# Optimization experiments

Hardware: AMD Instinct MI355X
Metric: run time of the kernel (lower is better)

Reference implementation:

```python
import jax, jax.numpy as jnp
import numpy as np

B, S, H, NH = 8, 512, 768, 12
HD = H // NH  # 64


def setup_inputs() -> dict:
    key = jax.random.key(0)
    ks = jax.random.split(key, 8)
    scale = 0.02
    return {
        "hidden_states": jax.random.normal(ks[0], (B, S, H), dtype=jnp.float32),
        "attention_mask": jnp.zeros((B, 1, 1, S), dtype=jnp.float32),
        "Wq": jax.random.normal(ks[1], (H, H), dtype=jnp.float32) * scale,
        "bq": jnp.zeros((H,), dtype=jnp.float32),
        "Wk": jax.random.normal(ks[2], (H, H), dtype=jnp.float32) * scale,
        "bk": jnp.zeros((H,), dtype=jnp.float32),
        "Wv": jax.random.normal(ks[3], (H, H), dtype=jnp.float32) * scale,
        "bv": jnp.zeros((H,), dtype=jnp.float32),
    }


def reference(hidden_states, attention_mask, Wq, bq, Wk, bk, Wv, bv):
    # BERT-style self-attention (dropout disabled / eval mode).
    def heads(x):  # [B,S,H] -> [B,NH,S,HD]
        return x.reshape(B, S, NH, HD).transpose(0, 2, 1, 3)

    q = heads(hidden_states @ Wq.T + bq)
    k = heads(hidden_states @ Wk.T + bk)
    v = heads(hidden_states @ Wv.T + bv)

    scores = jnp.einsum("bnqd,bnkd->bnqk", q, k) / jnp.sqrt(jnp.float32(HD))
    scores = scores + attention_mask  # additive mask broadcast over heads/queries
    probs = jax.nn.softmax(scores, axis=-1)
    ctx = jnp.einsum("bnqk,bnkd->bnqd", probs, v)
    return ctx.transpose(0, 2, 1, 3).reshape(B, S, H)
```

## Files before the change

kernel.cpp:

```cpp
#include <hip/hip_runtime.h>
#include <hip/hip_bf16.h>

typedef __bf16 bf16x8 __attribute__((ext_vector_type(8)));
typedef float f32x4 __attribute__((ext_vector_type(4)));
typedef float f32x16 __attribute__((ext_vector_type(16)));
typedef unsigned int u32x2 __attribute__((ext_vector_type(2)));
typedef unsigned int u32x4 __attribute__((ext_vector_type(4)));
typedef unsigned short us8 __attribute__((ext_vector_type(8)));

#define MFMA32(a, b, c) __builtin_amdgcn_mfma_f32_32x32x16_bf16((a), (b), (c), 0, 0, 0)

#define BATCH 8
#define SEQ 512
#define HID 768
#define NHEAD 12
#define HDIM 64

__device__ __forceinline__ unsigned short f2bf(float f) {
    unsigned int u = __float_as_uint(f);
    u += 0x7fffu + ((u >> 16) & 1u);
    return (unsigned short)(u >> 16);
}

__device__ __forceinline__ unsigned int cvtpk_bf16(float lo, float hi) {
    unsigned int r;
    asm("v_cvt_pk_bf16_f32 %0, %1, %2" : "=v"(r) : "v"(lo), "v"(hi));
    return r;
}

__global__ __launch_bounds__(256) void cvt_all_kernel(const float4* __restrict__ hs,
                                                      const float4* __restrict__ Wq,
                                                      const float4* __restrict__ Wk,
                                                      const float4* __restrict__ Wv,
                                                      unsigned short* __restrict__ hsb,
                                                      unsigned short* __restrict__ wb) {
    __shared__ us8 lds[768];

    const int tid = threadIdx.x;
    const int id = blockIdx.x;
    const int T = id >> 2;
    const int q = id & 3;

    const float4* src;
    int row0;
    unsigned short* dst;
    int Tout;
    if (T < 128) {
        src = hs; row0 = T * 32; dst = hsb; Tout = T;
    } else {
        int tw = T - 128;
        int which = tw / 24;
        src = (which == 0) ? Wq : ((which == 1) ? Wk : Wv);
        row0 = (tw - which * 24) * 32;
        dst = wb; Tout = tw;
    }

#pragma unroll
    for (int it = 0; it < 3; ++it) {
        int g = it * 256 + tid;
        int row = g / 24, ccl = g - row * 24;
        int fidx = (row0 + row) * 192 + (q * 24 + ccl) * 2;
        float4 v0 = src[fidx], v1 = src[fidx + 1];
        us8 o;
        o[0] = f2bf(v0.x); o[1] = f2bf(v0.y); o[2] = f2bf(v0.z); o[3] = f2bf(v0.w);
        o[4] = f2bf(v1.x); o[5] = f2bf(v1.y); o[6] = f2bf(v1.z); o[7] = f2bf(v1.w);
        int cell = row * 24 + ccl;
        lds[cell ^ (row & 7)] = o;
    }
    __syncthreads();

    const int w = tid >> 6, l = tid & 63;
    const int row = l & 31, h5 = l >> 5;
#pragma unroll
    for (int j = 0; j < 3; ++j) {
        int ktl = w * 3 + j;
        int kt = q * 12 + ktl;
        int cell = row * 24 + ktl * 2 + h5;
        us8 o = lds[cell ^ (row & 7)];
        *reinterpret_cast<us8*>(dst + ((size_t)Tout * 48 + kt) * 512 + l * 8) = o;
    }
}

__global__ __launch_bounds__(256) void qkv_gemm_kernel(const unsigned short* __restrict__ hsb,
                                                       const unsigned short* __restrict__ wb,
                                                       const float* __restrict__ bq,
                                                       const float* __restrict__ bk,
                                                       const float* __restrict__ bv,
                                                       unsigned short* __restrict__ Qf,
                                                       unsigned short* __restrict__ Kf,
                                                       unsigned short* __restrict__ VTf) {
    __shared__ __align__(16) char smem[49152];
    float* combine = (float*)smem;
    unsigned short* tb = (unsigned short*)smem;

    const int tid = threadIdx.x;
    const int w = tid >> 6;
    const int l = tid & 63;
    const int lq = l & 31, h5 = l >> 5;
    const int qn = w & 1;
    const int kh = w >> 1;

    const int id = blockIdx.x;
    const int xcd = id & 7, j = id >> 3;
    const int tm = (xcd >> 1) * 16 + j / 6;
    const int tn = (xcd & 1) * 6 + j % 6;

    const int fa0 = tm * 2;
    const int fb0 = tn * 6 + qn * 3;

    const unsigned short* paA = hsb + (size_t)fa0 * 48 * 512 + kh * 24 * 512 + l * 8;
    const unsigned short* paB = paA + 48 * 512;
    const unsigned short* pb0 = wb + (size_t)fb0 * 48 * 512 + kh * 24 * 512 + l * 8;
    const unsigned short* pb1 = pb0 + 48 * 512;
    const unsigned short* pb2 = pb1 + 48 * 512;

    f32x16 a00 = {}, a01 = {}, a02 = {}, a10 = {}, a11 = {}, a12 = {};

#pragma unroll 2
    for (int kt = 0; kt < 24; ++kt) {
        bf16x8 a0 = *reinterpret_cast<const bf16x8*>(paA + kt * 512);
        bf16x8 a1 = *reinterpret_cast<const bf16x8*>(paB + kt * 512);
        bf16x8 b0 = *reinterpret_cast<const bf16x8*>(pb0 + kt * 512);
        bf16x8 b1 = *reinterpret_cast<const bf16x8*>(pb1 + kt * 512);
        bf16x8 b2 = *reinterpret_cast<const bf16x8*>(pb2 + kt * 512);
        a00 = MFMA32(a0, b0, a00);
        a01 = MFMA32(a0, b1, a01);
        a02 = MFMA32(a0, b2, a02);
        a10 = MFMA32(a1, b0, a10);
        a11 = MFMA32(a1, b1, a11);
        a12 = MFMA32(a1, b2, a12);
    }

    f32x16 accs[2][3] = {{a00, a01, a02}, {a10, a11, a12}};

    if (kh == 1) {
#pragma unroll
        for (int mi = 0; mi < 2; ++mi)
#pragma unroll
            for (int ni = 0; ni < 3; ++ni)
#pragma unroll
                for (int r = 0; r < 16; ++r)
                    combine[((size_t)qn * 96 + (mi * 3 + ni) * 16 + r) * 64 + l] = accs[mi][ni][r];
    }
    __syncthreads();
    if (kh == 0) {
#pragma unroll
        for (int mi = 0; mi < 2; ++mi)
#pragma unroll
            for (int ni = 0; ni < 3; ++ni)
#pragma unroll
                for (int r = 0; r < 16; ++r)
                    accs[mi][ni][r] += combine[((size_t)qn * 96 + (mi * 3 + ni) * 16 + r) * 64 + l];
    }
    __syncthreads();

    const int which = tn / 4;
    const int b = tm >> 3;

    if (kh == 0) {
#pragma unroll
        for (int ni = 0; ni < 3; ++ni) {
            int d_local = qn * 96 + ni * 32 + lq;
            int col = tn * 192 + d_local;
            int oo = col - which * HID;
            const float* bias = (which == 0) ? bq : ((which == 1) ? bk : bv);
            float bvv = bias[oo];
            float scale = (which == 0) ? 0.125f : 1.0f;
#pragma unroll
            for (int mi = 0; mi < 2; ++mi) {
#pragma unroll
                for (int g = 0; g < 4; ++g) {
                    int s_base = mi * 32 + 8 * g + 4 * h5;
                    if (which == 2) {
                        ushort4 pk;
                        pk.x = f2bf(accs[mi][ni][4 * g + 0] + bvv);
                        pk.y = f2bf(accs[mi][ni][4 * g + 1] + bvv);
                        pk.z = f2bf(accs[mi][ni][4 * g + 2] + bvv);
                        pk.w = f2bf(accs[mi][ni][4 * g + 3] + bvv);
                        int byte = d_local * 128 + ((s_base * 2) ^ ((d_local & 7) << 4));
                        *reinterpret_cast<ushort4*>((char*)tb + byte) = pk;
                    } else {
#pragma unroll
                        for (int r2 = 0; r2 < 4; ++r2) {
                            int s_local = s_base + r2;
                            int dbyte = d_local * 2;
                            int byte = s_local * 384 + (dbyte & 0x180)
                                     + ((dbyte ^ ((s_local & 7) << 4)) & 0x7F);
                            *reinterpret_cast<unsigned short*>((char*)tb + byte) =
                                f2bf((accs[mi][ni][4 * g + r2] + bvv) * scale);
                        }
                    }
                }
            }
        }
    }
    __syncthreads();

    if (which != 2) {
        unsigned short* dstF = (which == 0) ? Qf : Kf;
        const int tnb = tn - which * 4;
#pragma unroll
        for (int j2 = 0; j2 < 6; ++j2) {
            int fi = w * 6 + j2;
            int dc = fi & 3;
            int t2 = fi >> 2;
            int hl = t2 % 3, qt_l = t2 / 3;
            int head = tnb * 3 + hl;
            int qt = (tm & 7) * 2 + qt_l;
            int s_local = qt_l * 32 + lq;
            int dbyte = (hl * 64 + dc * 16 + h5 * 8) * 2;
            int byte = s_local * 384 + (dbyte & 0x180)
                     + ((dbyte ^ ((s_local & 7) << 4)) & 0x7F);
            us8 v = *reinterpret_cast<const us8*>((char*)tb + byte);
            size_t off = ((((size_t)(b * NHEAD + head)) * 16 + qt) * 4 + dc) * 512 + l * 8;
            *reinterpret_cast<us8*>(dstF + off) = v;
        }
    } else {
#pragma unroll
        for (int j2 = 0; j2 < 6; ++j2) {
            int fi = w * 6 + j2;
            int kt2l = fi & 3;
            int t2 = fi >> 2;
            int hl = t2 % 3, nt = t2 / 3;
            int head = (tn - 8) * 3 + hl;
            int d_local = hl * 64 + nt * 32 + lq;
            int sbyte = kt2l * 32 + h5 * 16;
            int byte = d_local * 128 + (sbyte ^ ((d_local & 7) << 4));
            us8 v = *reinterpret_cast<const us8*>((char*)tb + byte);
            int kt2 = (tm & 7) * 4 + kt2l;
            size_t off = ((((size_t)(b * NHEAD + head)) * 2 + nt) * 32 + kt2) * 512 + l * 8;
            *reinterpret_cast<us8*>(VTf + off) = v;
        }
    }
}

__global__ __launch_bounds__(256, 3) void attn_kernel(const unsigned short* __restrict__ Qf,
                                                      const unsigned short* __restrict__ Kf,
                                                      const unsigned short* __restrict__ VTf,
                                                      const float* __restrict__ mask,
                                                      float* __restrict__ out) {
    __shared__ float lds_ctx[2][32][64];
    __shared__ float lds_den[2][32];

    const int tid = threadIdx.x;
    const int w = tid >> 6;
    const int l = tid & 63;
    const int lq = l & 31;
    const int h5 = l >> 5;
    const int qg = w & 1;
    const int kh = w >> 1;

    const int id = blockIdx.x;
    const int hh = id % 96;
    const int qb = id / 96;
    const int b = hh / 12;
    const int hd = hh % 12;

    const int bh = b * NHEAD + hd;
    const int q0 = qb * 64 + qg * 32;
    const float4* mask4 = (const float4*)mask;

    bf16x8 qf[4];
    {
        const unsigned short* qbase = Qf + (((size_t)bh * 16 + (qb * 2 + qg)) * 4) * 512 + l * 8;
#pragma unroll
        for (int dc = 0; dc < 4; ++dc)
            qf[dc] = *reinterpret_cast<const bf16x8*>(qbase + dc * 512);
    }

    const unsigned short* kbase  = Kf + (((size_t)bh * 16 + kh * 8) * 4) * 512 + l * 8;
    const unsigned short* vbase0 = VTf + (((size_t)bh * 2 + 0) * 32 + kh * 16) * 512 + l * 8;
    const unsigned short* vbase1 = VTf + (((size_t)bh * 2 + 1) * 32 + kh * 16) * 512 + l * 8;

    f32x16 ctx0 = {};
    f32x16 ctx1 = {};
    float den = 0.f;

#pragma unroll
    for (int kb = 0; kb < 8; ++kb) {
        bf16x8 kf[4];
#pragma unroll
        for (int dc = 0; dc < 4; ++dc)
            kf[dc] = *reinterpret_cast<const bf16x8*>(kbase + (kb * 4 + dc) * 512);

        f32x16 T = {};
#pragma unroll
        for (int dc = 0; dc < 4; ++dc)
            T = MFMA32(kf[dc], qf[dc], T);

        bf16x8 vf00 = *reinterpret_cast<const bf16x8*>(vbase0 + kb * 2 * 512);
        bf16x8 vf10 = *reinterpret_cast<const bf16x8*>(vbase0 + (kb * 2 + 1) * 512);
        bf16x8 vf01 = *reinterpret_cast<const bf16x8*>(vbase1 + kb * 2 * 512);
        bf16x8 vf11 = *reinterpret_cast<const bf16x8*>(vbase1 + (kb * 2 + 1) * 512);

        const int k0 = kh * 256 + kb * 32;
        float4 mv[4];
#pragma unroll
        for (int g = 0; g < 4; ++g)
            mv[g] = mask4[b * 128 + (k0 >> 2) + 2 * g + h5];

        float p[16];
#pragma unroll
        for (int r = 0; r < 16; ++r) {
            float mval = (r & 3) == 0 ? mv[r >> 2].x : ((r & 3) == 1 ? mv[r >> 2].y
                       : ((r & 3) == 2 ? mv[r >> 2].z : mv[r >> 2].w));
            p[r] = __expf(T[r] + mval);
            den += p[r];
        }

        bf16x8 pa[2];
#pragma unroll
        for (int c = 0; c < 2; ++c) {
            int base = c * 8;
            unsigned int lo01 = cvtpk_bf16(p[base + 0], p[base + 1]);
            unsigned int lo23 = cvtpk_bf16(p[base + 2], p[base + 3]);
            unsigned int hi01 = cvtpk_bf16(p[base + 4], p[base + 5]);
            unsigned int hi23 = cvtpk_bf16(p[base + 6], p[base + 7]);
            u32x2 s1 = __builtin_amdgcn_permlane32_swap(lo01, hi01, false, false);
            u32x2 s2 = __builtin_amdgcn_permlane32_swap(lo23, hi23, false, false);
            u32x4 words = {s1[0], s2[0], s1[1], s2[1]};
            pa[c] = __builtin_bit_cast(bf16x8, words);
        }

        ctx0 = MFMA32(pa[0], vf00, ctx0);
        ctx0 = MFMA32(pa[1], vf10, ctx0);
        ctx1 = MFMA32(pa[0], vf01, ctx1);
        ctx1 = MFMA32(pa[1], vf11, ctx1);
    }

    float den_full = den + __shfl_xor(den, 32);

    if (kh == 1) {
        if (l < 32) lds_den[qg][l] = den_full;
#pragma unroll
        for (int r = 0; r < 16; ++r) {
            int qr = (r & 3) + 8 * (r >> 2) + 4 * h5;
            lds_ctx[qg][qr][lq] = ctx0[r];
            lds_ctx[qg][qr][32 + lq] = ctx1[r];
        }
    }
    __syncthreads();
    if (kh == 0) {
        float den_tot = den_full + lds_den[qg][lq];
#pragma unroll
        for (int r = 0; r < 16; ++r) {
            int qr = (r & 3) + 8 * (r >> 2) + 4 * h5;
            float dn = 1.0f / __shfl(den_tot, qr);
            size_t rowoff = ((size_t)b * SEQ + q0 + qr) * HID + hd * HDIM;
            out[rowoff + lq]      = (ctx0[r] + lds_ctx[qg][qr][lq]) * dn;
            out[rowoff + 32 + lq] = (ctx1[r] + lds_ctx[qg][qr][32 + lq]) * dn;
        }
    }
}

extern "C" void kernel_launch(void* const* d_in, const int* in_sizes, int n_in,
                              void* d_out, int out_size, void* d_ws, size_t ws_size,
                              hipStream_t stream) {
    const float* hs   = (const float*)d_in[0];
    const float* mask = (const float*)d_in[1];
    const float* Wq   = (const float*)d_in[2];
    const float* bq   = (const float*)d_in[3];
    const float* Wk   = (const float*)d_in[4];
    const float* bk   = (const float*)d_in[5];
    const float* Wv   = (const float*)d_in[6];
    const float* bv   = (const float*)d_in[7];
    float* out = (float*)d_out;

    char* ws = (char*)d_ws;
    unsigned short* hsb = (unsigned short*)(ws);
    unsigned short* wb  = (unsigned short*)(ws + 6291456);
    unsigned short* Qf  = (unsigned short*)(ws + 9830400);
    unsigned short* Kf  = (unsigned short*)(ws + 16121856);
    unsigned short* VTf = (unsigned short*)(ws + 22413312);

    cvt_all_kernel<<<800, 256, 0, stream>>>((const float4*)hs, (const float4*)Wq,
                                            (const float4*)Wk, (const float4*)Wv,
                                            hsb, wb);
    qkv_gemm_kernel<<<768, 256, 0, stream>>>(hsb, wb, bq, bk, bv, Qf, Kf, VTf);
    attn_kernel<<<768, 256, 0, stream>>>(Qf, Kf, VTf, mask, out);
}
```

Measured before the change: 56.15 us.

## Split attention key range across four waves per 32-query block

Each attention block now handles a single 32-query tile with four waves, each covering a quarter of the keys (128), instead of two query tiles times two key halves. The grid doubles to 1536 blocks, and partial contexts and denominators from three waves are reduced through LDS by wave 0. The goal is shorter per-wave serial loops and more parallelism to hide latency, at the cost of more LDS reduction traffic, more total Q loads, and an idle-heavy epilogue in which only one wave writes output.

```diff
diff --git a/kernel.cpp b/kernel.cpp
--- a/kernel.cpp
+++ b/kernel.cpp
@@ -234,50 +234,48 @@
     }
 }
 
-__global__ __launch_bounds__(256, 3) void attn_kernel(const unsigned short* __restrict__ Qf,
-                                                      const unsigned short* __restrict__ Kf,
-                                                      const unsigned short* __restrict__ VTf,
-                                                      const float* __restrict__ mask,
-                                                      float* __restrict__ out) {
-    __shared__ float lds_ctx[2][32][64];
-    __shared__ float lds_den[2][32];
+__global__ __launch_bounds__(256) void attn_kernel(const unsigned short* __restrict__ Qf,
+                                                   const unsigned short* __restrict__ Kf,
+                                                   const unsigned short* __restrict__ VTf,
+                                                   const float* __restrict__ mask,
+                                                   float* __restrict__ out) {
+    __shared__ float lds_ctx[3][32][64];
+    __shared__ float lds_den[3][32];
 
     const int tid = threadIdx.x;
     const int w = tid >> 6;
     const int l = tid & 63;
     const int lq = l & 31;
     const int h5 = l >> 5;
-    const int qg = w & 1;
-    const int kh = w >> 1;
 
     const int id = blockIdx.x;
     const int hh = id % 96;
-    const int qb = id / 96;
+    const int qg = id / 96;
     const int b = hh / 12;
     const int hd = hh % 12;
 
     const int bh = b * NHEAD + hd;
-    const int q0 = qb * 64 + qg * 32;
+    const int q0 = qg * 32;
     const float4* mask4 = (const float4*)mask;
 
     bf16x8 qf[4];
     {
-        const unsigned short* qbase = Qf + (((size_t)bh * 16 + (qb * 2 + qg)) * 4) * 512 + l * 8;
+        const unsigned short* qbase = Qf + (((size_t)bh * 16 + qg) * 4) * 512 + l * 8;
 #pragma unroll
         for (int dc = 0; dc < 4; ++dc)
             qf[dc] = *reinterpret_cast<const bf16x8*>(qbase + dc * 512);
     }
 
-    const unsigned short* kbase  = Kf + (((size_t)bh * 16 + kh * 8) * 4) * 512 + l * 8;
-    const unsigned short* vbase0 = VTf + (((size_t)bh * 2 + 0) * 32 + kh * 16) * 512 + l * 8;
-    const unsigned short* vbase1 = VTf + (((size_t)bh * 2 + 1) * 32 + kh * 16) * 512 + l * 8;
+    const unsigned short* kbase  = Kf + (((size_t)bh * 16 + w * 4) * 4) * 512 + l * 8;
+    const unsigned short* vbase0 = VTf + (((size_t)bh * 2 + 0) * 32 + w * 8) * 512 + l * 8;
+    const unsigned short* vbase1 = VTf + (((size_t)bh * 2 + 1) * 32 + w * 8) * 512 + l * 8;
 
     f32x16 ctx0 = {};
     f32x16 ctx1 = {};
     float den = 0.f;
 
 #pragma unroll
-    for (int kb = 0; kb < 8; ++kb) {
+    for (int kb = 0; kb < 4; ++kb) {
         bf16x8 kf[4];
 #pragma unroll
         for (int dc = 0; dc < 4; ++dc)
@@ -293,7 +291,7 @@
         bf16x8 vf01 = *reinterpret_cast<const bf16x8*>(vbase1 + kb * 2 * 512);
         bf16x8 vf11 = *reinterpret_cast<const bf16x8*>(vbase1 + (kb * 2 + 1) * 512);
 
-        const int k0 = kh * 256 + kb * 32;
+        const int k0 = w * 128 + kb * 32;
         float4 mv[4];
 #pragma unroll
         for (int g = 0; g < 4; ++g)
@@ -330,25 +328,27 @@
 
     float den_full = den + __shfl_xor(den, 32);
 
-    if (kh == 1) {
-        if (l < 32) lds_den[qg][l] = den_full;
+    if (w > 0) {
+        if (l < 32) lds_den[w - 1][l] = den_full;
 #pragma unroll
         for (int r = 0; r < 16; ++r) {
             int qr = (r & 3) + 8 * (r >> 2) + 4 * h5;
-            lds_ctx[qg][qr][lq] = ctx0[r];
-            lds_ctx[qg][qr][32 + lq] = ctx1[r];
-        }
-    }
-    __syncthreads();
-    if (kh == 0) {
-        float den_tot = den_full + lds_den[qg][lq];
+            lds_ctx[w - 1][qr][lq] = ctx0[r];
+            lds_ctx[w - 1][qr][32 + lq] = ctx1[r];
+        }
+    }
+    __syncthreads();
+    if (w == 0) {
+        float den_tot = den_full + lds_den[0][lq] + lds_den[1][lq] + lds_den[2][lq];
 #pragma unroll
         for (int r = 0; r < 16; ++r) {
             int qr = (r & 3) + 8 * (r >> 2) + 4 * h5;
             float dn = 1.0f / __shfl(den_tot, qr);
             size_t rowoff = ((size_t)b * SEQ + q0 + qr) * HID + hd * HDIM;
-            out[rowoff + lq]      = (ctx0[r] + lds_ctx[qg][qr][lq]) * dn;
-            out[rowoff + 32 + lq] = (ctx1[r] + lds_ctx[qg][qr][32 + lq]) * dn;
+            out[rowoff + lq] = (ctx0[r] + lds_ctx[0][qr][lq] + lds_ctx[1][qr][lq]
+                                + lds_ctx[2][qr][lq]) * dn;
+            out[rowoff + 32 + lq] = (ctx1[r] + lds_ctx[0][qr][32 + lq] + lds_ctx[1][qr][32 + lq]
+                                     + lds_ctx[2][qr][32 + lq]) * dn;
         }
     }
 }
@@ -377,5 +377,5 @@
                                             (const float4*)Wk, (const float4*)Wv,
                                             hsb, wb);
     qkv_gemm_kernel<<<768, 256, 0, stream>>>(hsb, wb, bq, bk, bv, Qf, Kf, VTf);
-    attn_kernel<<<768, 256, 0, stream>>>(Qf, Kf, VTf, mask, out);
-}
+    attn_kernel<<<1536, 256, 0, stream>>>(Qf, Kf, VTf, mask, out);
+}
```

After: 55.75 us. About the same (-0.7%).
